# Optimization experiments

Measured on AMD Instinct MI355X. Metric: run time of the kernel, lower is better.

## Reference

```python
import jax, jax.numpy as jnp
import numpy as np

HEADS = 8
DIM_HEAD = 64
SCALE = DIM_HEAD ** -0.5


def setup_inputs() -> dict:
    key = jax.random.key(0)
    ks = jax.random.split(key, 6)
    B, N, D = 4, 2048, 512
    inner = HEADS * DIM_HEAD  # 512
    x = jax.random.normal(ks[0], (B, N, D), dtype=jnp.float32)
    centroid_delta = jax.random.normal(ks[1], (B, 3, N, N), dtype=jnp.float32)
    Wqkv = jax.random.normal(ks[2], (D, 3 * inner), dtype=jnp.float32) * (D ** -0.5)
    Wout = jax.random.normal(ks[3], (inner, D), dtype=jnp.float32) * (inner ** -0.5)
    bout = jnp.zeros((D,), dtype=jnp.float32)
    rel_w = jax.random.normal(ks[4], (HEADS, 3), dtype=jnp.float32)
    rel_b = jnp.zeros((HEADS,), dtype=jnp.float32)
    return {"x": x, "centroid_delta": centroid_delta, "Wqkv": Wqkv,
            "Wout": Wout, "bout": bout, "rel_w": rel_w, "rel_b": rel_b}


def reference(x, centroid_delta, Wqkv, Wout, bout, rel_w, rel_b):
    B, N, D = x.shape
    h, d = HEADS, DIM_HEAD
    qkv = x @ Wqkv                      # [B, N, 3*h*d]
    q, k, v = jnp.split(qkv, 3, axis=-1)
    # [B, N, h*d] -> [B, h, N, d]
    reshape = lambda t: t.reshape(B, N, h, d).transpose(0, 2, 1, 3)
    q, k, v = reshape(q), reshape(k), reshape(v)
    dots = jnp.einsum('bhid,bhjd->bhij', q, k) * SCALE  # [B, h, N, N]
    # 1x1 conv: Conv2d(3, heads, 1) on centroid_delta [B, 3, N, N]
    bias = jnp.einsum('hc,bcij->bhij', rel_w, centroid_delta) + rel_b[None, :, None, None]
    attn = jax.nn.softmax(dots + bias, axis=-1)
    out = jnp.einsum('bhij,bhjd->bhid', attn, v)        # [B, h, N, d]
    out = out.transpose(0, 2, 1, 3).reshape(B, N, h * d)
    return out @ Wout + bout
```

## Files before the change

kernel.cpp:

```cpp
#include <hip/hip_runtime.h>
#include <hip/hip_bf16.h>

typedef __bf16 bf16_t;
typedef __bf16 bf16x8 __attribute__((ext_vector_type(8)));
typedef float f32x4 __attribute__((ext_vector_type(4)));

#define SCALE_ 0.125f
#define BATCH 4
#define NSEQ 2048
#define DMODEL 512
#define HEADS 8
#define DHEAD 64
#define QKVN 1536
#define NN (NSEQ * NSEQ)

__global__ __launch_bounds__(256) void cvt_bf16_kernel(const float* __restrict__ in,
                                                       bf16_t* __restrict__ out, int n4) {
  int i = blockIdx.x * 256 + threadIdx.x;
  if (i < n4) {
    float4 v = ((const float4*)in)[i];
    union { bf16_t b[4]; uint2 u; } pk;
    pk.b[0] = (bf16_t)v.x; pk.b[1] = (bf16_t)v.y;
    pk.b[2] = (bf16_t)v.z; pk.b[3] = (bf16_t)v.w;
    ((uint2*)out)[i] = pk.u;
  }
}

__global__ __launch_bounds__(256) void cvt_transpose_kernel(const float* __restrict__ in,
                                                            bf16_t* __restrict__ out, int R, int C) {
  int i = blockIdx.x * 256 + threadIdx.x;
  if (i < R * C) {
    int cc = i / R, rr = i - cc * R;
    out[(size_t)cc * R + rr] = (bf16_t)in[(size_t)rr * C + cc];
  }
}

template<int BIAS, int OUTF32>
__global__ __launch_bounds__(256) void gemm_bt_kernel(const bf16_t* __restrict__ A,
    const bf16_t* __restrict__ Bt, void* __restrict__ Cout,
    const float* __restrict__ bias, int M, int N, int K) {
  __shared__ __align__(16) bf16_t As[64][72];
  __shared__ __align__(16) bf16_t Bs[64][72];
  const int tid = threadIdx.x;
  const int w = tid >> 6, lane = tid & 63, quad = lane >> 4, l16 = lane & 15;
  const int m0 = blockIdx.x * 64, n0 = blockIdx.y * 64;
  const int sr = tid >> 3, sg = tid & 7;
  f32x4 acc[4] = {};
  for (int k0 = 0; k0 < K; k0 += 64) {
    *(uint4*)&As[sr][sg * 8]      = *(const uint4*)&A[(size_t)(m0 + sr) * K + k0 + sg * 8];
    *(uint4*)&As[sr + 32][sg * 8] = *(const uint4*)&A[(size_t)(m0 + sr + 32) * K + k0 + sg * 8];
    *(uint4*)&Bs[sr][sg * 8]      = *(const uint4*)&Bt[(size_t)(n0 + sr) * K + k0 + sg * 8];
    *(uint4*)&Bs[sr + 32][sg * 8] = *(const uint4*)&Bt[(size_t)(n0 + sr + 32) * K + k0 + sg * 8];
    __syncthreads();
    bf16x8 a0 = *(const bf16x8*)&As[w * 16 + l16][quad * 8];
    bf16x8 a1 = *(const bf16x8*)&As[w * 16 + l16][32 + quad * 8];
#pragma unroll
    for (int nt = 0; nt < 4; nt++) {
      bf16x8 b0 = *(const bf16x8*)&Bs[nt * 16 + l16][quad * 8];
      bf16x8 b1 = *(const bf16x8*)&Bs[nt * 16 + l16][32 + quad * 8];
      acc[nt] = __builtin_amdgcn_mfma_f32_16x16x32_bf16(a0, b0, acc[nt], 0, 0, 0);
      acc[nt] = __builtin_amdgcn_mfma_f32_16x16x32_bf16(a1, b1, acc[nt], 0, 0, 0);
    }
    __syncthreads();
  }
#pragma unroll
  for (int nt = 0; nt < 4; nt++) {
    int col = n0 + nt * 16 + l16;
    float bv = BIAS ? bias[col] : 0.0f;
#pragma unroll
    for (int rr = 0; rr < 4; rr++) {
      int row = m0 + w * 16 + quad * 4 + rr;
      float v = acc[nt][rr] + bv;
      if (OUTF32) ((float*)Cout)[(size_t)row * N + col] = v;
      else        ((bf16_t*)Cout)[(size_t)row * N + col] = (bf16_t)v;
    }
  }
}

__global__ __launch_bounds__(256, 4) void attn_kernel(const bf16_t* __restrict__ qkv,
    const float* __restrict__ cd, const float* __restrict__ rel_w,
    const float* __restrict__ rel_b, bf16_t* __restrict__ ao) {
  __shared__ __align__(16) bf16_t Ks[64][72];
  __shared__ __align__(16) bf16_t Vts[64][72];
  __shared__ __align__(16) bf16_t Ps[64][72];
  const int tid = threadIdx.x;
  const int w = tid >> 6, lane = tid & 63, quad = lane >> 4, l16 = lane & 15;
  const int bid = blockIdx.x;
  const int h = bid >> 7, b = (bid >> 5) & 3, it = bid & 31;

  const size_t qoff = (size_t)(b * NSEQ + it * 64 + w * 16 + l16) * QKVN + h * DHEAD;
  bf16x8 q0 = *(const bf16x8*)&qkv[qoff + quad * 8];
  bf16x8 q1 = *(const bf16x8*)&qkv[qoff + 32 + quad * 8];

  const float rw0 = rel_w[h * 3 + 0], rw1 = rel_w[h * 3 + 1], rw2 = rel_w[h * 3 + 2];
  const float rb = rel_b[h];

  f32x4 o[4] = {};
  float m_r[4], l_r[4];
#pragma unroll
  for (int r = 0; r < 4; r++) { m_r[r] = -1e30f; l_r[r] = 0.0f; }

  const int sr = tid >> 3, sg = tid & 7;
  const size_t kbase = (size_t)b * NSEQ * QKVN + DMODEL + h * DHEAD;

  const int row0 = it * 64 + w * 16 + quad * 4;
  const float* cdp = cd + (size_t)b * 3 * NN + (size_t)row0 * NSEQ + l16;

  float cdr[3][4][4];
#pragma unroll
  for (int ch = 0; ch < 3; ch++)
#pragma unroll
    for (int ct = 0; ct < 4; ct++)
#pragma unroll
      for (int r = 0; r < 4; r++)
        cdr[ch][ct][r] = cdp[ch * NN + r * NSEQ + ct * 16];

  for (int jt = 0; jt < 32; jt++) {
#pragma unroll
    for (int rep = 0; rep < 2; rep++) {
      int jrel = sr + rep * 32;
      const bf16_t* kptr = &qkv[kbase + (size_t)(jt * 64 + jrel) * QKVN + sg * 8];
      *(uint4*)&Ks[jrel][sg * 8] = *(const uint4*)kptr;
      union { bf16_t b[8]; uint4 u; } vt;
      vt.u = *(const uint4*)(kptr + DMODEL);
      const int pc = jrel ^ ((sg & 3) << 3);
#pragma unroll
      for (int e = 0; e < 8; e++) Vts[sg * 8 + e][pc] = vt.b[e];
    }
    __syncthreads();

    f32x4 s[4] = {};
#pragma unroll
    for (int ct = 0; ct < 4; ct++) {
      bf16x8 b0 = *(const bf16x8*)&Ks[ct * 16 + l16][quad * 8];
      bf16x8 b1 = *(const bf16x8*)&Ks[ct * 16 + l16][32 + quad * 8];
      s[ct] = __builtin_amdgcn_mfma_f32_16x16x32_bf16(q0, b0, s[ct], 0, 0, 0);
      s[ct] = __builtin_amdgcn_mfma_f32_16x16x32_bf16(q1, b1, s[ct], 0, 0, 0);
    }

#pragma unroll
    for (int ct = 0; ct < 4; ct++)
#pragma unroll
      for (int r = 0; r < 4; r++)
        s[ct][r] = s[ct][r] * SCALE_ +
                   (rw0 * cdr[0][ct][r] + rw1 * cdr[1][ct][r] + rw2 * cdr[2][ct][r] + rb);

    {
      const int jb = (jt < 31 ? jt + 1 : jt) * 64;
#pragma unroll
      for (int ch = 0; ch < 3; ch++)
#pragma unroll
        for (int ct = 0; ct < 4; ct++)
#pragma unroll
          for (int r = 0; r < 4; r++)
            cdr[ch][ct][r] = cdp[ch * NN + r * NSEQ + jb + ct * 16];
    }

#pragma unroll
    for (int r = 0; r < 4; r++) {
      float mx = fmaxf(fmaxf(s[0][r], s[1][r]), fmaxf(s[2][r], s[3][r]));
#pragma unroll
      for (int off = 8; off >= 1; off >>= 1) mx = fmaxf(mx, __shfl_xor(mx, off, 64));
      float mnew = fmaxf(m_r[r], mx);
      float alpha = __expf(m_r[r] - mnew);
      float rsum = 0.0f;
#pragma unroll
      for (int ct = 0; ct < 4; ct++) {
        float p = __expf(s[ct][r] - mnew);
        s[ct][r] = p; rsum += p;
      }
#pragma unroll
      for (int off = 8; off >= 1; off >>= 1) rsum += __shfl_xor(rsum, off, 64);
      l_r[r] = l_r[r] * alpha + rsum;
      m_r[r] = mnew;
#pragma unroll
      for (int dt = 0; dt < 4; dt++) o[dt][r] *= alpha;
    }

#pragma unroll
    for (int ct = 0; ct < 4; ct++)
#pragma unroll
      for (int rr = 0; rr < 4; rr++)
        Ps[w * 16 + quad * 4 + rr][(ct * 16 + l16) ^ (quad << 3)] = (bf16_t)s[ct][rr];

    const int psw = ((l16 >> 2) & 3) << 3;
    bf16x8 p0 = *(const bf16x8*)&Ps[w * 16 + l16][(quad * 8) ^ psw];
    bf16x8 p1 = *(const bf16x8*)&Ps[w * 16 + l16][32 + ((quad * 8) ^ psw)];
#pragma unroll
    for (int dt = 0; dt < 4; dt++) {
      const int row = dt * 16 + l16;
      const int vsw = ((row >> 3) & 3) << 3;
      bf16x8 v0 = *(const bf16x8*)&Vts[row][(quad * 8) ^ vsw];
      bf16x8 v1 = *(const bf16x8*)&Vts[row][32 + ((quad * 8) ^ vsw)];
      o[dt] = __builtin_amdgcn_mfma_f32_16x16x32_bf16(p0, v0, o[dt], 0, 0, 0);
      o[dt] = __builtin_amdgcn_mfma_f32_16x16x32_bf16(p1, v1, o[dt], 0, 0, 0);
    }
    __syncthreads();
  }

#pragma unroll
  for (int dt = 0; dt < 4; dt++) {
    int col = h * DHEAD + dt * 16 + l16;
#pragma unroll
    for (int rr = 0; rr < 4; rr++) {
      int row = b * NSEQ + it * 64 + w * 16 + quad * 4 + rr;
      ao[(size_t)row * DMODEL + col] = (bf16_t)(o[dt][rr] / l_r[rr]);
    }
  }
}

extern "C" void kernel_launch(void* const* d_in, const int* in_sizes, int n_in,
                              void* d_out, int out_size, void* d_ws, size_t ws_size,
                              hipStream_t stream) {
  const float* x     = (const float*)d_in[0];
  const float* cd    = (const float*)d_in[1];
  const float* Wqkv  = (const float*)d_in[2];
  const float* Wout  = (const float*)d_in[3];
  const float* bout  = (const float*)d_in[4];
  const float* rel_w = (const float*)d_in[5];
  const float* rel_b = (const float*)d_in[6];
  float* out = (float*)d_out;

  char* ws = (char*)d_ws;
  const size_t M = (size_t)BATCH * NSEQ;
  bf16_t* xb    = (bf16_t*)ws;
  bf16_t* WqkvT = (bf16_t*)(ws + 8388608);
  bf16_t* WoutT = (bf16_t*)(ws + 8388608 + 1572864);
  bf16_t* qkv   = (bf16_t*)(ws + 8388608 + 1572864 + 524288);
  bf16_t* ao    = (bf16_t*)(ws + 8388608 + 1572864 + 524288 + 25165824);

  cvt_bf16_kernel<<<(int)(M * DMODEL / 4 / 256), 256, 0, stream>>>(x, xb, (int)(M * DMODEL / 4));
  cvt_transpose_kernel<<<(DMODEL * QKVN) / 256, 256, 0, stream>>>(Wqkv, WqkvT, DMODEL, QKVN);
  cvt_transpose_kernel<<<(DMODEL * DMODEL) / 256, 256, 0, stream>>>(Wout, WoutT, DMODEL, DMODEL);

  gemm_bt_kernel<0, 0><<<dim3(M / 64, QKVN / 64), 256, 0, stream>>>(
      xb, WqkvT, (void*)qkv, nullptr, (int)M, QKVN, DMODEL);

  attn_kernel<<<BATCH * 32 * HEADS, 256, 0, stream>>>(qkv, cd, rel_w, rel_b, ao);

  gemm_bt_kernel<1, 1><<<dim3(M / 64, DMODEL / 64), 256, 0, stream>>>(
      ao, WoutT, (void*)out, bout, (int)M, DMODEL, DMODEL);
}
```

Measured before the change: 512.2 us.

## Enlarge GEMM tiles with direct-to-LDS loads, prefetch K/V and fold bias early

The projection GEMMs move to 128x128 tiles with a swizzled LDS layout filled by global_load_lds, so each loaded element is reused more and fewer blocks are launched. The weight transpose now goes through a shared-memory tile so that reads and writes are coalesced. In the attention kernel the next K/V tile is prefetched into registers while the current one is computed, and the three-channel relative bias is folded into one value per element at load time, which cuts register use. The cost is more registers per GEMM thread and fewer blocks for the output GEMM. The attention kernel's time is still set by the large centroid_delta read.

```diff
diff --git a/kernel.cpp b/kernel.cpp
--- a/kernel.cpp
+++ b/kernel.cpp
@@ -12,7 +12,18 @@
 #define HEADS 8
 #define DHEAD 64
 #define QKVN 1536
-#define NN (NSEQ * NSEQ)
+#define NN ((size_t)NSEQ * NSEQ)
+
+#define BAR() asm volatile("s_waitcnt lgkmcnt(0)\n\ts_barrier" ::: "memory")
+
+__device__ __forceinline__ void gload_lds16(const void* g, void* l) {
+  __builtin_amdgcn_global_load_lds((const __attribute__((address_space(1))) void*)g,
+                                   (__attribute__((address_space(3))) void*)l, 16, 0, 0);
+}
+
+__device__ __forceinline__ f32x4 mfma16(bf16x8 a, bf16x8 b, f32x4 c) {
+  return __builtin_amdgcn_mfma_f32_16x16x32_bf16(a, b, c, 0, 0, 0);
+}
 
 __global__ __launch_bounds__(256) void cvt_bf16_kernel(const float* __restrict__ in,
                                                        bf16_t* __restrict__ out, int n4) {
@@ -28,51 +39,84 @@
 
 __global__ __launch_bounds__(256) void cvt_transpose_kernel(const float* __restrict__ in,
                                                             bf16_t* __restrict__ out, int R, int C) {
-  int i = blockIdx.x * 256 + threadIdx.x;
-  if (i < R * C) {
-    int cc = i / R, rr = i - cc * R;
-    out[(size_t)cc * R + rr] = (bf16_t)in[(size_t)rr * C + cc];
+  __shared__ float tile[64][65];
+  const int r0 = blockIdx.y * 64, c0 = blockIdx.x * 64;
+  const int tx = threadIdx.x & 63, tg = threadIdx.x >> 6;
+#pragma unroll
+  for (int i = 0; i < 16; i++) {
+    int rr = tg * 16 + i;
+    tile[rr][tx] = in[(size_t)(r0 + rr) * C + c0 + tx];
+  }
+  __syncthreads();
+#pragma unroll
+  for (int i = 0; i < 16; i++) {
+    int cc = tg * 16 + i;
+    out[(size_t)(c0 + cc) * R + r0 + tx] = (bf16_t)tile[tx][cc];
   }
 }
 
 template<int BIAS, int OUTF32>
-__global__ __launch_bounds__(256) void gemm_bt_kernel(const bf16_t* __restrict__ A,
+__global__ __launch_bounds__(256) void gemm128_kernel(const bf16_t* __restrict__ A,
     const bf16_t* __restrict__ Bt, void* __restrict__ Cout,
     const float* __restrict__ bias, int M, int N, int K) {
-  __shared__ __align__(16) bf16_t As[64][72];
-  __shared__ __align__(16) bf16_t Bs[64][72];
+  __shared__ __align__(16) bf16_t As[128 * 64];
+  __shared__ __align__(16) bf16_t Bs[128 * 64];
   const int tid = threadIdx.x;
   const int w = tid >> 6, lane = tid & 63, quad = lane >> 4, l16 = lane & 15;
-  const int m0 = blockIdx.x * 64, n0 = blockIdx.y * 64;
-  const int sr = tid >> 3, sg = tid & 7;
-  f32x4 acc[4] = {};
+  const int wm = w & 1, wn = w >> 1;
+  const int m0 = blockIdx.x * 128, n0 = blockIdx.y * 128;
+  f32x4 acc[4][4] = {};
+  int srow[4], scg[4];
+#pragma unroll
+  for (int t = 0; t < 4; t++) {
+    int s = (w * 4 + t) * 64 + lane;
+    srow[t] = s >> 3;
+    scg[t] = (s & 7) ^ (srow[t] & 7);
+  }
   for (int k0 = 0; k0 < K; k0 += 64) {
-    *(uint4*)&As[sr][sg * 8]      = *(const uint4*)&A[(size_t)(m0 + sr) * K + k0 + sg * 8];
-    *(uint4*)&As[sr + 32][sg * 8] = *(const uint4*)&A[(size_t)(m0 + sr + 32) * K + k0 + sg * 8];
-    *(uint4*)&Bs[sr][sg * 8]      = *(const uint4*)&Bt[(size_t)(n0 + sr) * K + k0 + sg * 8];
-    *(uint4*)&Bs[sr + 32][sg * 8] = *(const uint4*)&Bt[(size_t)(n0 + sr + 32) * K + k0 + sg * 8];
+#pragma unroll
+    for (int t = 0; t < 4; t++) {
+      gload_lds16(&A[(size_t)(m0 + srow[t]) * K + k0 + scg[t] * 8], &As[(w * 4 + t) * 512]);
+      gload_lds16(&Bt[(size_t)(n0 + srow[t]) * K + k0 + scg[t] * 8], &Bs[(w * 4 + t) * 512]);
+    }
     __syncthreads();
-    bf16x8 a0 = *(const bf16x8*)&As[w * 16 + l16][quad * 8];
-    bf16x8 a1 = *(const bf16x8*)&As[w * 16 + l16][32 + quad * 8];
+    bf16x8 af[4][2], bfr[4][2];
+#pragma unroll
+    for (int mt = 0; mt < 4; mt++) {
+      int row = wm * 64 + mt * 16 + l16;
+#pragma unroll
+      for (int kh = 0; kh < 2; kh++)
+        af[mt][kh] = *(const bf16x8*)&As[(row * 8 + ((kh * 4 + quad) ^ (row & 7))) * 8];
+    }
 #pragma unroll
     for (int nt = 0; nt < 4; nt++) {
-      bf16x8 b0 = *(const bf16x8*)&Bs[nt * 16 + l16][quad * 8];
-      bf16x8 b1 = *(const bf16x8*)&Bs[nt * 16 + l16][32 + quad * 8];
-      acc[nt] = __builtin_amdgcn_mfma_f32_16x16x32_bf16(a0, b0, acc[nt], 0, 0, 0);
-      acc[nt] = __builtin_amdgcn_mfma_f32_16x16x32_bf16(a1, b1, acc[nt], 0, 0, 0);
-    }
+      int row = wn * 64 + nt * 16 + l16;
+#pragma unroll
+      for (int kh = 0; kh < 2; kh++)
+        bfr[nt][kh] = *(const bf16x8*)&Bs[(row * 8 + ((kh * 4 + quad) ^ (row & 7))) * 8];
+    }
+#pragma unroll
+    for (int mt = 0; mt < 4; mt++)
+#pragma unroll
+      for (int nt = 0; nt < 4; nt++) {
+        acc[mt][nt] = mfma16(af[mt][0], bfr[nt][0], acc[mt][nt]);
+        acc[mt][nt] = mfma16(af[mt][1], bfr[nt][1], acc[mt][nt]);
+      }
     __syncthreads();
   }
 #pragma unroll
   for (int nt = 0; nt < 4; nt++) {
-    int col = n0 + nt * 16 + l16;
+    int col = n0 + wn * 64 + nt * 16 + l16;
     float bv = BIAS ? bias[col] : 0.0f;
 #pragma unroll
-    for (int rr = 0; rr < 4; rr++) {
-      int row = m0 + w * 16 + quad * 4 + rr;
-      float v = acc[nt][rr] + bv;
-      if (OUTF32) ((float*)Cout)[(size_t)row * N + col] = v;
-      else        ((bf16_t*)Cout)[(size_t)row * N + col] = (bf16_t)v;
+    for (int mt = 0; mt < 4; mt++) {
+#pragma unroll
+      for (int rr = 0; rr < 4; rr++) {
+        int row = m0 + wm * 64 + mt * 16 + quad * 4 + rr;
+        float v = acc[mt][nt][rr] + bv;
+        if (OUTF32) ((float*)Cout)[(size_t)row * N + col] = v;
+        else        ((bf16_t*)Cout)[(size_t)row * N + col] = (bf16_t)v;
+      }
     }
   }
 }
@@ -105,56 +149,58 @@
 
   const int row0 = it * 64 + w * 16 + quad * 4;
   const float* cdp = cd + (size_t)b * 3 * NN + (size_t)row0 * NSEQ + l16;
-
-  float cdr[3][4][4];
-#pragma unroll
-  for (int ch = 0; ch < 3; ch++)
-#pragma unroll
-    for (int ct = 0; ct < 4; ct++)
-#pragma unroll
-      for (int r = 0; r < 4; r++)
-        cdr[ch][ct][r] = cdp[ch * NN + r * NSEQ + ct * 16];
+  float biasr[4][4];
+#define LOADBIAS(JT) do { const int jb_ = (JT) * 64;                                   \
+  _Pragma("unroll") for (int ct_ = 0; ct_ < 4; ct_++)                                  \
+  _Pragma("unroll") for (int r_ = 0; r_ < 4; r_++) {                                   \
+    size_t ci_ = (size_t)r_ * NSEQ + jb_ + ct_ * 16;                                   \
+    biasr[ct_][r_] = fmaf(rw0, cdp[ci_],                                               \
+                     fmaf(rw1, cdp[ci_ + NN], fmaf(rw2, cdp[ci_ + 2 * NN], rb)));      \
+  } } while (0)
+
+  uint4 k0r, k1r, v0r, v1r;
+  {
+    const bf16_t* p = &qkv[kbase + (size_t)sr * QKVN + sg * 8];
+    k0r = *(const uint4*)p;               v0r = *(const uint4*)(p + DMODEL);
+    k1r = *(const uint4*)(p + 32 * QKVN); v1r = *(const uint4*)(p + 32 * QKVN + DMODEL);
+  }
+  LOADBIAS(0);
 
   for (int jt = 0; jt < 32; jt++) {
-#pragma unroll
-    for (int rep = 0; rep < 2; rep++) {
-      int jrel = sr + rep * 32;
-      const bf16_t* kptr = &qkv[kbase + (size_t)(jt * 64 + jrel) * QKVN + sg * 8];
-      *(uint4*)&Ks[jrel][sg * 8] = *(const uint4*)kptr;
-      union { bf16_t b[8]; uint4 u; } vt;
-      vt.u = *(const uint4*)(kptr + DMODEL);
-      const int pc = jrel ^ ((sg & 3) << 3);
-#pragma unroll
-      for (int e = 0; e < 8; e++) Vts[sg * 8 + e][pc] = vt.b[e];
-    }
-    __syncthreads();
+    *(uint4*)&Ks[sr][sg * 8]      = k0r;
+    *(uint4*)&Ks[sr + 32][sg * 8] = k1r;
+    {
+      union { bf16_t e[8]; uint4 u; } va, vb; va.u = v0r; vb.u = v1r;
+      const int pc = sr ^ ((sg & 3) << 3);
+#pragma unroll
+      for (int e2 = 0; e2 < 8; e2++) {
+        Vts[sg * 8 + e2][pc]      = va.e[e2];
+        Vts[sg * 8 + e2][pc + 32] = vb.e[e2];
+      }
+    }
+    BAR();
+
+    if (jt < 31) {
+      const bf16_t* p = &qkv[kbase + (size_t)((jt + 1) * 64 + sr) * QKVN + sg * 8];
+      k0r = *(const uint4*)p;               v0r = *(const uint4*)(p + DMODEL);
+      k1r = *(const uint4*)(p + 32 * QKVN); v1r = *(const uint4*)(p + 32 * QKVN + DMODEL);
+    }
 
     f32x4 s[4] = {};
 #pragma unroll
     for (int ct = 0; ct < 4; ct++) {
       bf16x8 b0 = *(const bf16x8*)&Ks[ct * 16 + l16][quad * 8];
       bf16x8 b1 = *(const bf16x8*)&Ks[ct * 16 + l16][32 + quad * 8];
-      s[ct] = __builtin_amdgcn_mfma_f32_16x16x32_bf16(q0, b0, s[ct], 0, 0, 0);
-      s[ct] = __builtin_amdgcn_mfma_f32_16x16x32_bf16(q1, b1, s[ct], 0, 0, 0);
+      s[ct] = mfma16(q0, b0, s[ct]);
+      s[ct] = mfma16(q1, b1, s[ct]);
     }
 
 #pragma unroll
     for (int ct = 0; ct < 4; ct++)
 #pragma unroll
       for (int r = 0; r < 4; r++)
-        s[ct][r] = s[ct][r] * SCALE_ +
-                   (rw0 * cdr[0][ct][r] + rw1 * cdr[1][ct][r] + rw2 * cdr[2][ct][r] + rb);
-
-    {
-      const int jb = (jt < 31 ? jt + 1 : jt) * 64;
-#pragma unroll
-      for (int ch = 0; ch < 3; ch++)
-#pragma unroll
-        for (int ct = 0; ct < 4; ct++)
-#pragma unroll
-          for (int r = 0; r < 4; r++)
-            cdr[ch][ct][r] = cdp[ch * NN + r * NSEQ + jb + ct * 16];
-    }
+        s[ct][r] = s[ct][r] * SCALE_ + biasr[ct][r];
+    if (jt < 31) LOADBIAS(jt + 1);
 
 #pragma unroll
     for (int r = 0; r < 4; r++) {
@@ -192,10 +238,10 @@
       const int vsw = ((row >> 3) & 3) << 3;
       bf16x8 v0 = *(const bf16x8*)&Vts[row][(quad * 8) ^ vsw];
       bf16x8 v1 = *(const bf16x8*)&Vts[row][32 + ((quad * 8) ^ vsw)];
-      o[dt] = __builtin_amdgcn_mfma_f32_16x16x32_bf16(p0, v0, o[dt], 0, 0, 0);
-      o[dt] = __builtin_amdgcn_mfma_f32_16x16x32_bf16(p1, v1, o[dt], 0, 0, 0);
-    }
-    __syncthreads();
+      o[dt] = mfma16(p0, v0, o[dt]);
+      o[dt] = mfma16(p1, v1, o[dt]);
+    }
+    BAR();
   }
 
 #pragma unroll
@@ -207,6 +253,7 @@
       ao[(size_t)row * DMODEL + col] = (bf16_t)(o[dt][rr] / l_r[rr]);
     }
   }
+#undef LOADBIAS
 }
 
 extern "C" void kernel_launch(void* const* d_in, const int* in_sizes, int n_in,
@@ -230,14 +277,14 @@
   bf16_t* ao    = (bf16_t*)(ws + 8388608 + 1572864 + 524288 + 25165824);
 
   cvt_bf16_kernel<<<(int)(M * DMODEL / 4 / 256), 256, 0, stream>>>(x, xb, (int)(M * DMODEL / 4));
-  cvt_transpose_kernel<<<(DMODEL * QKVN) / 256, 256, 0, stream>>>(Wqkv, WqkvT, DMODEL, QKVN);
-  cvt_transpose_kernel<<<(DMODEL * DMODEL) / 256, 256, 0, stream>>>(Wout, WoutT, DMODEL, DMODEL);
-
-  gemm_bt_kernel<0, 0><<<dim3(M / 64, QKVN / 64), 256, 0, stream>>>(
+  cvt_transpose_kernel<<<dim3(QKVN / 64, DMODEL / 64), 256, 0, stream>>>(Wqkv, WqkvT, DMODEL, QKVN);
+  cvt_transpose_kernel<<<dim3(DMODEL / 64, DMODEL / 64), 256, 0, stream>>>(Wout, WoutT, DMODEL, DMODEL);
+
+  gemm128_kernel<0, 0><<<dim3(M / 128, QKVN / 128), 256, 0, stream>>>(
       xb, WqkvT, (void*)qkv, nullptr, (int)M, QKVN, DMODEL);
 
   attn_kernel<<<BATCH * 32 * HEADS, 256, 0, stream>>>(qkv, cd, rel_w, rel_b, ao);
 
-  gemm_bt_kernel<1, 1><<<dim3(M / 64, DMODEL / 64), 256, 0, stream>>>(
+  gemm128_kernel<1, 1><<<dim3(M / 128, DMODEL / 128), 256, 0, stream>>>(
       ao, WoutT, (void*)out, bout, (int)M, DMODEL, DMODEL);
 }
```

After: 443.8 us. 1.15x faster.
